# Kernel tuning notes

Hardware: AMD Instinct MI355X
Metric: run time of the kernel (lower is better)

## Reference

```python
import jax, jax.numpy as jnp
import numpy as np
from jax import lax

INF = 1e6  # stand-in for infinity; INF**2 = 1e12 fits comfortably in fp32


def _boundary_3x3(targets):
    """morphological_gradient(size=(3,3)) > 0 on int label maps [B,H,W].
    scipy default mode='reflect' with pad width 1 == edge padding."""
    B, H, W = targets.shape
    p = jnp.pad(targets, ((0, 0), (1, 1), (1, 1)), mode='edge')
    patches = jnp.stack([p[:, i:i + H, j:j + W]
                         for i in range(3) for j in range(3)], axis=0)
    return (patches.max(0) - patches.min(0)) > 0  # [B,H,W] bool


def _row_dist(boundary):
    """Per-row 1D distance (in column index) to nearest boundary pixel. [B,H,W] float."""
    B, H, W = boundary.shape
    bT = jnp.moveaxis(boundary, 2, 0)  # [W,B,H]

    def step(c, b):
        c = jnp.where(b, 0.0, jnp.minimum(c + 1.0, INF))
        return c, c

    init = jnp.full((B, H), INF, dtype=jnp.float32)
    _, fwd = lax.scan(step, init, bT)
    _, bwd = lax.scan(step, init, bT[::-1])
    g = jnp.minimum(fwd, bwd[::-1])  # [W,B,H]
    return jnp.moveaxis(g, 0, 2)  # [B,H,W]


def _edt(boundary):
    """Exact 2D Euclidean distance transform to the boundary set (separable form):
    d(i,j)^2 = min_k ( (i-k)^2 + g(k,j)^2 )."""
    B, H, W = boundary.shape
    g2 = _row_dist(boundary) ** 2  # [B,H,W]
    ii = jnp.arange(H, dtype=jnp.float32)
    dk2 = (ii[:, None] - ii[None, :]) ** 2  # [H_i, H_k]
    # [B, H_i, H_k, W] -> min over k
    d2 = jnp.min(dk2[None, :, :, None] + g2[:, None, :, :], axis=2)
    return jnp.sqrt(d2)


def boundary_weight(targets, sigma):
    boundary = _boundary_3x3(targets)
    dist = _edt(boundary)
    w = jnp.exp(-dist / sigma)
    has_b = boundary.any(axis=(1, 2))[:, None, None]
    return jnp.where(has_b, w, 1.0)  # all-ones map if no boundary


def setup_inputs() -> dict:
    key = jax.random.key(0)
    k1, k2 = jax.random.split(key)
    B, C, H, W = 8, 19, 256, 256
    inputs = jax.random.normal(k1, (B, C, H, W), dtype=jnp.float32)
    targets = jax.random.randint(k2, (B, H, W), 0, C, dtype=jnp.int32)
    return {"inputs": inputs, "targets": targets}


def reference(inputs, targets):
    sigma = 5.0
    logp = jax.nn.log_softmax(inputs, axis=1)  # [B,C,H,W]
    ce = -jnp.take_along_axis(logp, targets[:, None, :, :], axis=1)[:, 0]  # [B,H,W]
    w = boundary_weight(targets, sigma)
    return (ce * w).mean()
```

## Files before the change

### kernel.cpp

```cpp
#include <hip/hip_runtime.h>

#define BB 8
#define CC 19
#define HH 256
#define WW 256
#define HWW 65536
#define IT 8
#define BIGF 3.0e12f


__global__ __launch_bounds__(256) void k_bnd_ce(
    const float* __restrict__ x, const int* __restrict__ tgt,
    float* __restrict__ g2, float* __restrict__ ce,
    int* __restrict__ rowany, float* __restrict__ out)
{
    const int blk = blockIdx.x;
    const int b   = blk >> 6;
    const int i0  = (blk & 63) << 2;
    const int j   = threadIdx.x;

    __shared__ int trow[6][WW];
    __shared__ int bflag[4][WW];
    __shared__ int s_any;

    if (blk == 0 && j == 0) out[0] = 0.0f;
    if (j == 0) s_any = 0;

    const int* tbase = tgt + b * HWW;
#pragma unroll
    for (int rr = 0; rr < 6; ++rr) {
        int hh = min(max(i0 - 1 + rr, 0), HH - 1);
        trow[rr][j] = tbase[hh * WW + j];
    }
    __syncthreads();

    const int r  = j >> 6;
    const int c0 = (j & 63) << 2;
    const int h  = i0 + r;

    int anyb = 0;
#pragma unroll
    for (int t = 0; t < 4; ++t) {
        int c = c0 + t;
        int cm = max(c - 1, 0), cp = min(c + 1, WW - 1);
        int mx = trow[r][cm], mn = mx;
#pragma unroll
        for (int rr = 0; rr < 3; ++rr) {
            int a0 = trow[r + rr][cm], a1 = trow[r + rr][c], a2 = trow[r + rr][cp];
            mx = max(mx, max(a0, max(a1, a2)));
            mn = min(mn, min(a0, min(a1, a2)));
        }
        int bnd = (mx != mn) ? 1 : 0;
        bflag[r][c] = bnd;
        anyb |= bnd;
    }
    unsigned long long msk = __ballot(anyb);
    if ((j & 63) == 0 && msk) s_any = 1;
    __syncthreads();
    if (j == 0) rowany[blk] = s_any;

    float4 g4;
    float* gp = (float*)&g4;
#pragma unroll
    for (int t = 0; t < 4; ++t) {
        int c = c0 + t;
        float mind = 1e6f;
        for (int d = 0; d < WW; ++d) {
            int lo = c - d, hi = c + d;
            if ((lo >= 0 && bflag[r][lo]) || (hi < WW && bflag[r][hi])) {
                mind = (float)d; break;
            }
        }
        gp[t] = mind * mind;
    }
    *(float4*)(g2 + (size_t)(b * HH + h) * WW + c0) = g4;

    const float* px = x + ((size_t)(b * CC) * HH + h) * WW + c0;
    float4 s4 = make_float4(0.f, 0.f, 0.f, 0.f);
#pragma unroll
    for (int c = 0; c < CC; ++c) {
        float4 v = *(const float4*)(px + (size_t)c * HWW);
        s4.x += expf(v.x); s4.y += expf(v.y);
        s4.z += expf(v.z); s4.w += expf(v.w);
    }
    const int t0 = trow[r + 1][c0],     t1 = trow[r + 1][c0 + 1],
              t2 = trow[r + 1][c0 + 2], t3 = trow[r + 1][c0 + 3];
    float4 c4;
    c4.x = logf(s4.x) - px[(size_t)t0 * HWW + 0];
    c4.y = logf(s4.y) - px[(size_t)t1 * HWW + 1];
    c4.z = logf(s4.z) - px[(size_t)t2 * HWW + 2];
    c4.w = logf(s4.w) - px[(size_t)t3 * HWW + 3];
    *(float4*)(ce + (size_t)(b * HH + h) * WW + c0) = c4;
}

__global__ __launch_bounds__(256) void k_edt_red(
    const float* __restrict__ g2, const float* __restrict__ ce,
    const int* __restrict__ rowany, float* __restrict__ out)
{
    const int b  = blockIdx.x >> 5;
    const int i0 = (blockIdx.x & 31) * IT;
    const int j  = threadIdx.x;

    __shared__ int s_has;
    __shared__ float wsum[4];
    if (j == 0) s_has = 0;
    int ra = (j < 64) ? rowany[b * 64 + j] : 0;
    unsigned long long mk = __ballot(ra != 0);
    __syncthreads();
    if ((j & 63) == 0 && mk) s_has = 1;
    __syncthreads();
    const int has = s_has;

    float md[IT];
#pragma unroll
    for (int r = 0; r < IT; ++r) md[r] = BIGF;
    const float* gcol = g2 + (size_t)b * HWW + j;
    const int c0 = i0 + 4;
    for (int d0 = 0; d0 < HH; d0 += 4) {
        float gl[4], gr[4];
        int   kl[4], kr[4];
#pragma unroll
        for (int t = 0; t < 4; ++t) {
            int d = d0 + t;
            kl[t] = c0 - d; kr[t] = c0 + d;
            gl[t] = (kl[t] >= 0 && kl[t] < HH) ? gcol[(size_t)kl[t] * WW] : BIGF;
            gr[t] = (kr[t] >= 0 && kr[t] < HH) ? gcol[(size_t)kr[t] * WW] : BIGF;
        }
#pragma unroll
        for (int t = 0; t < 4; ++t) {
#pragma unroll
            for (int r = 0; r < IT; ++r) {
                float dl = (float)(i0 + r - kl[t]);
                float dr = (float)(i0 + r - kr[t]);
                md[r] = fminf(md[r], fmaf(dl, dl, gl[t]));
                md[r] = fminf(md[r], fmaf(dr, dr, gr[t]));
            }
        }
        float bm = md[0];
#pragma unroll
        for (int r = 1; r < IT; ++r) bm = fmaxf(bm, md[r]);
        float fut = (float)(d0 * d0);
        if (fut > bm) break;
    }

    float acc = 0.0f;
#pragma unroll
    for (int r = 0; r < IT; ++r) {
        float dist = sqrtf(md[r]);
        float w = has ? expf(-dist / 5.0f) : 1.0f;
        acc += ce[((size_t)b * HH + i0 + r) * WW + j] * w;
    }

    for (int off = 32; off > 0; off >>= 1)
        acc += __shfl_down(acc, off, 64);
    const int lane = j & 63, wid = j >> 6;
    if (lane == 0) wsum[wid] = acc;
    __syncthreads();
    if (j == 0) {
        float tot = wsum[0] + wsum[1] + wsum[2] + wsum[3];
        atomicAdd(out, tot * (1.0f / (float)(BB * HWW)));
    }
}

extern "C" void kernel_launch(void* const* d_in, const int* in_sizes, int n_in,
                              void* d_out, int out_size, void* d_ws, size_t ws_size,
                              hipStream_t stream) {
    const float* x   = (const float*)d_in[0];
    const int*   tgt = (const int*)d_in[1];
    float*       out = (float*)d_out;

    char* ws = (char*)d_ws;
    float* g2     = (float*)ws;
    float* ce     = (float*)(ws + (size_t)BB * HWW * sizeof(float));
    int*   rowany = (int*)  (ws + (size_t)2 * BB * HWW * sizeof(float));

    k_bnd_ce <<<BB * (HH / 4), 256, 0, stream>>>(x, tgt, g2, ce, rowany, out);
    k_edt_red<<<BB * (HH / IT), 256, 0, stream>>>(g2, ce, rowany, out);
}
```

Baseline: 86.99 us.

## Double threads in boundary/CE kernel and prefetch logits before boundary work

```diff
diff --git a/kernel.cpp b/kernel.cpp
--- a/kernel.cpp
+++ b/kernel.cpp
@@ -9,7 +9,7 @@
 #define BIGF 3.0e12f
 
 
-__global__ __launch_bounds__(256) void k_bnd_ce(
+__global__ __launch_bounds__(512, 4) void k_bnd_ce(
     const float* __restrict__ x, const int* __restrict__ tgt,
     float* __restrict__ g2, float* __restrict__ ce,
     int* __restrict__ rowany, float* __restrict__ out)
@@ -26,21 +26,36 @@
     if (blk == 0 && j == 0) out[0] = 0.0f;
     if (j == 0) s_any = 0;
 
+    const int r  = j >> 7;
+    const int c0 = (j & 127) << 1;
+    const int h  = i0 + r;
+
     const int* tbase = tgt + b * HWW;
+    int tv[3];
 #pragma unroll
-    for (int rr = 0; rr < 6; ++rr) {
+    for (int k = 0; k < 3; ++k) {
+        int idx = j + (k << 9);
+        int rr = idx >> 8, cc = idx & 255;
         int hh = min(max(i0 - 1 + rr, 0), HH - 1);
-        trow[rr][j] = tbase[hh * WW + j];
+        tv[k] = tbase[hh * WW + cc];
+    }
+
+    const float* px = x + ((size_t)(b * CC) * HH + h) * WW + c0;
+    float2 v[CC];
+#pragma unroll
+    for (int c = 0; c < CC; ++c)
+        v[c] = *(const float2*)(px + (size_t)c * HWW);
+
+#pragma unroll
+    for (int k = 0; k < 3; ++k) {
+        int idx = j + (k << 9);
+        trow[idx >> 8][idx & 255] = tv[k];
     }
     __syncthreads();
 
-    const int r  = j >> 6;
-    const int c0 = (j & 63) << 2;
-    const int h  = i0 + r;
-
     int anyb = 0;
 #pragma unroll
-    for (int t = 0; t < 4; ++t) {
+    for (int t = 0; t < 2; ++t) {
         int c = c0 + t;
         int cm = max(c - 1, 0), cp = min(c + 1, WW - 1);
         int mx = trow[r][cm], mn = mx;
@@ -59,10 +74,9 @@
     __syncthreads();
     if (j == 0) rowany[blk] = s_any;
 
-    float4 g4;
-    float* gp = (float*)&g4;
+    float gv[2];
 #pragma unroll
-    for (int t = 0; t < 4; ++t) {
+    for (int t = 0; t < 2; ++t) {
         int c = c0 + t;
         float mind = 1e6f;
         for (int d = 0; d < WW; ++d) {
@@ -71,26 +85,20 @@
                 mind = (float)d; break;
             }
         }
-        gp[t] = mind * mind;
+        gv[t] = mind * mind;
     }
-    *(float4*)(g2 + (size_t)(b * HH + h) * WW + c0) = g4;
+    *(float2*)(g2 + (size_t)(b * HH + h) * WW + c0) = make_float2(gv[0], gv[1]);
 
-    const float* px = x + ((size_t)(b * CC) * HH + h) * WW + c0;
-    float4 s4 = make_float4(0.f, 0.f, 0.f, 0.f);
+    const int t0 = trow[r + 1][c0], t1 = trow[r + 1][c0 + 1];
+    float sx = 0.0f, sy = 0.0f, xv0 = 0.0f, xv1 = 0.0f;
 #pragma unroll
     for (int c = 0; c < CC; ++c) {
-        float4 v = *(const float4*)(px + (size_t)c * HWW);
-        s4.x += expf(v.x); s4.y += expf(v.y);
-        s4.z += expf(v.z); s4.w += expf(v.w);
+        sx += expf(v[c].x); sy += expf(v[c].y);
+        xv0 = (c == t0) ? v[c].x : xv0;
+        xv1 = (c == t1) ? v[c].y : xv1;
     }
-    const int t0 = trow[r + 1][c0],     t1 = trow[r + 1][c0 + 1],
-              t2 = trow[r + 1][c0 + 2], t3 = trow[r + 1][c0 + 3];
-    float4 c4;
-    c4.x = logf(s4.x) - px[(size_t)t0 * HWW + 0];
-    c4.y = logf(s4.y) - px[(size_t)t1 * HWW + 1];
-    c4.z = logf(s4.z) - px[(size_t)t2 * HWW + 2];
-    c4.w = logf(s4.w) - px[(size_t)t3 * HWW + 3];
-    *(float4*)(ce + (size_t)(b * HH + h) * WW + c0) = c4;
+    *(float2*)(ce + (size_t)(b * HH + h) * WW + c0) =
+        make_float2(logf(sx) - xv0, logf(sy) - xv1);
 }
 
 __global__ __launch_bounds__(256) void k_edt_red(
@@ -174,6 +182,6 @@
     float* ce     = (float*)(ws + (size_t)BB * HWW * sizeof(float));
     int*   rowany = (int*)  (ws + (size_t)2 * BB * HWW * sizeof(float));
 
-    k_bnd_ce <<<BB * (HH / 4), 256, 0, stream>>>(x, tgt, g2, ce, rowany, out);
+    k_bnd_ce <<<BB * (HH / 4), 512, 0, stream>>>(x, tgt, g2, ce, rowany, out);
     k_edt_red<<<BB * (HH / IT), 256, 0, stream>>>(g2, ce, rowany, out);
 }
```

Result: no change. 87.30 us (+0.4%).

## Prefetch logits before boundary work and shrink blocks in both kernels

Applied to the files above, without the earlier changes.

```diff
diff --git a/kernel.cpp b/kernel.cpp
--- a/kernel.cpp
+++ b/kernel.cpp
@@ -5,38 +5,53 @@
 #define HH 256
 #define WW 256
 #define HWW 65536
-#define IT 8
+#define IT 4
 #define BIGF 3.0e12f
 
 
-__global__ __launch_bounds__(256) void k_bnd_ce(
+__global__ __launch_bounds__(128, 4) void k_bnd_ce(
     const float* __restrict__ x, const int* __restrict__ tgt,
     float* __restrict__ g2, float* __restrict__ ce,
     int* __restrict__ rowany, float* __restrict__ out)
 {
     const int blk = blockIdx.x;
-    const int b   = blk >> 6;
-    const int i0  = (blk & 63) << 2;
+    const int b   = blk >> 7;
+    const int i0  = (blk & 127) << 1;
     const int j   = threadIdx.x;
 
-    __shared__ int trow[6][WW];
-    __shared__ int bflag[4][WW];
+    __shared__ int trow[4][WW];
+    __shared__ int bflag[2][WW];
     __shared__ int s_any;
 
     if (blk == 0 && j == 0) out[0] = 0.0f;
     if (j == 0) s_any = 0;
 
-    const int* tbase = tgt + b * HWW;
-#pragma unroll
-    for (int rr = 0; rr < 6; ++rr) {
-        int hh = min(max(i0 - 1 + rr, 0), HH - 1);
-        trow[rr][j] = tbase[hh * WW + j];
-    }
-    __syncthreads();
-
     const int r  = j >> 6;
     const int c0 = (j & 63) << 2;
     const int h  = i0 + r;
+
+    const int* tbase = tgt + b * HWW;
+    int tv[8];
+#pragma unroll
+    for (int k = 0; k < 8; ++k) {
+        int idx = j + (k << 7);
+        int rr = idx >> 8, cc = idx & 255;
+        int hh = min(max(i0 - 1 + rr, 0), HH - 1);
+        tv[k] = tbase[hh * WW + cc];
+    }
+
+    const float* px = x + ((size_t)(b * CC) * HH + h) * WW + c0;
+    float4 v[CC];
+#pragma unroll
+    for (int c = 0; c < CC; ++c)
+        v[c] = *(const float4*)(px + (size_t)c * HWW);
+
+#pragma unroll
+    for (int k = 0; k < 8; ++k) {
+        int idx = j + (k << 7);
+        trow[idx >> 8][idx & 255] = tv[k];
+    }
+    __syncthreads();
 
     int anyb = 0;
 #pragma unroll
@@ -75,21 +90,24 @@
     }
     *(float4*)(g2 + (size_t)(b * HH + h) * WW + c0) = g4;
 
-    const float* px = x + ((size_t)(b * CC) * HH + h) * WW + c0;
+    const int t0 = trow[r + 1][c0],     t1 = trow[r + 1][c0 + 1],
+              t2 = trow[r + 1][c0 + 2], t3 = trow[r + 1][c0 + 3];
     float4 s4 = make_float4(0.f, 0.f, 0.f, 0.f);
+    float xv0 = 0.f, xv1 = 0.f, xv2 = 0.f, xv3 = 0.f;
 #pragma unroll
     for (int c = 0; c < CC; ++c) {
-        float4 v = *(const float4*)(px + (size_t)c * HWW);
-        s4.x += expf(v.x); s4.y += expf(v.y);
-        s4.z += expf(v.z); s4.w += expf(v.w);
+        s4.x += expf(v[c].x); s4.y += expf(v[c].y);
+        s4.z += expf(v[c].z); s4.w += expf(v[c].w);
+        xv0 = (c == t0) ? v[c].x : xv0;
+        xv1 = (c == t1) ? v[c].y : xv1;
+        xv2 = (c == t2) ? v[c].z : xv2;
+        xv3 = (c == t3) ? v[c].w : xv3;
     }
-    const int t0 = trow[r + 1][c0],     t1 = trow[r + 1][c0 + 1],
-              t2 = trow[r + 1][c0 + 2], t3 = trow[r + 1][c0 + 3];
     float4 c4;
-    c4.x = logf(s4.x) - px[(size_t)t0 * HWW + 0];
-    c4.y = logf(s4.y) - px[(size_t)t1 * HWW + 1];
-    c4.z = logf(s4.z) - px[(size_t)t2 * HWW + 2];
-    c4.w = logf(s4.w) - px[(size_t)t3 * HWW + 3];
+    c4.x = logf(s4.x) - xv0;
+    c4.y = logf(s4.y) - xv1;
+    c4.z = logf(s4.z) - xv2;
+    c4.w = logf(s4.w) - xv3;
     *(float4*)(ce + (size_t)(b * HH + h) * WW + c0) = c4;
 }
 
@@ -97,14 +115,14 @@
     const float* __restrict__ g2, const float* __restrict__ ce,
     const int* __restrict__ rowany, float* __restrict__ out)
 {
-    const int b  = blockIdx.x >> 5;
-    const int i0 = (blockIdx.x & 31) * IT;
+    const int b  = blockIdx.x >> 6;
+    const int i0 = (blockIdx.x & 63) * IT;
     const int j  = threadIdx.x;
 
     __shared__ int s_has;
     __shared__ float wsum[4];
     if (j == 0) s_has = 0;
-    int ra = (j < 64) ? rowany[b * 64 + j] : 0;
+    int ra = (j < 128) ? rowany[b * 128 + j] : 0;
     unsigned long long mk = __ballot(ra != 0);
     __syncthreads();
     if ((j & 63) == 0 && mk) s_has = 1;
@@ -115,7 +133,7 @@
 #pragma unroll
     for (int r = 0; r < IT; ++r) md[r] = BIGF;
     const float* gcol = g2 + (size_t)b * HWW + j;
-    const int c0 = i0 + 4;
+    const int c0 = i0 + 2;
     for (int d0 = 0; d0 < HH; d0 += 4) {
         float gl[4], gr[4];
         int   kl[4], kr[4];
@@ -174,6 +192,6 @@
     float* ce     = (float*)(ws + (size_t)BB * HWW * sizeof(float));
     int*   rowany = (int*)  (ws + (size_t)2 * BB * HWW * sizeof(float));
 
-    k_bnd_ce <<<BB * (HH / 4), 256, 0, stream>>>(x, tgt, g2, ce, rowany, out);
+    k_bnd_ce <<<BB * (HH / 2), 128, 0, stream>>>(x, tgt, g2, ce, rowany, out);
     k_edt_red<<<BB * (HH / IT), 256, 0, stream>>>(g2, ce, rowany, out);
 }
```

Measured after the change: 93.42 us. +7.4%, slower.

## Fuse boundary/CE and EDT reduction into one cooperative grid-synced kernel

Applied to the files above, without the earlier changes.

```diff
diff --git a/kernel.cpp b/kernel.cpp
--- a/kernel.cpp
+++ b/kernel.cpp
@@ -1,13 +1,164 @@
 #include <hip/hip_runtime.h>
+#include <hip/hip_cooperative_groups.h>
+
+namespace cg = cooperative_groups;
 
 #define BB 8
 #define CC 19
 #define HH 256
 #define WW 256
 #define HWW 65536
-#define IT 8
 #define BIGF 3.0e12f
-
+#define SENT 1.0e11f
+
+
+__global__ __launch_bounds__(256) void k_fused(
+    const float* __restrict__ x, const int* __restrict__ tgt,
+    float* __restrict__ g2, float* __restrict__ out)
+{
+    const int blk = blockIdx.x;
+    const int b   = blk >> 6;
+    const int i0  = (blk & 63) << 2;
+    const int j   = threadIdx.x;
+
+    __shared__ int   trow[6][WW];
+    __shared__ int   bflag[4][WW];
+    __shared__ float gsh[4][WW];
+    __shared__ float wsum[4];
+
+    if (blk == 0 && j == 0) out[0] = 0.0f;
+
+    const int* tbase = tgt + b * HWW;
+#pragma unroll
+    for (int rr = 0; rr < 6; ++rr) {
+        int hh = min(max(i0 - 1 + rr, 0), HH - 1);
+        trow[rr][j] = tbase[hh * WW + j];
+    }
+
+    const int r  = j >> 6;
+    const int c0 = (j & 63) << 2;
+    const int h  = i0 + r;
+
+    const float* px = x + ((size_t)(b * CC) * HH + h) * WW + c0;
+    float4 v[CC];
+#pragma unroll
+    for (int c = 0; c < CC; ++c)
+        v[c] = *(const float4*)(px + (size_t)c * HWW);
+
+    __syncthreads();
+
+#pragma unroll
+    for (int t = 0; t < 4; ++t) {
+        int c = c0 + t;
+        int cm = max(c - 1, 0), cp = min(c + 1, WW - 1);
+        int mx = trow[r][cm], mn = mx;
+#pragma unroll
+        for (int rr = 0; rr < 3; ++rr) {
+            int a0 = trow[r + rr][cm], a1 = trow[r + rr][c], a2 = trow[r + rr][cp];
+            mx = max(mx, max(a0, max(a1, a2)));
+            mn = min(mn, min(a0, min(a1, a2)));
+        }
+        bflag[r][c] = (mx != mn) ? 1 : 0;
+    }
+    __syncthreads();
+
+    float4 g4;
+    float* gp = (float*)&g4;
+#pragma unroll
+    for (int t = 0; t < 4; ++t) {
+        int c = c0 + t;
+        float mind = 1e6f;
+        for (int d = 0; d < WW; ++d) {
+            int lo = c - d, hi = c + d;
+            if ((lo >= 0 && bflag[r][lo]) || (hi < WW && bflag[r][hi])) {
+                mind = (float)d; break;
+            }
+        }
+        gp[t] = mind * mind;
+    }
+    *(float4*)&gsh[r][c0] = g4;
+    *(float4*)(g2 + (size_t)(b * HH + h) * WW + c0) = g4;
+
+    const int t0 = trow[r + 1][c0],     t1 = trow[r + 1][c0 + 1],
+              t2 = trow[r + 1][c0 + 2], t3 = trow[r + 1][c0 + 3];
+    float4 s4 = make_float4(0.f, 0.f, 0.f, 0.f);
+    float xv0 = 0.f, xv1 = 0.f, xv2 = 0.f, xv3 = 0.f;
+#pragma unroll
+    for (int c = 0; c < CC; ++c) {
+        s4.x += expf(v[c].x); s4.y += expf(v[c].y);
+        s4.z += expf(v[c].z); s4.w += expf(v[c].w);
+        xv0 = (c == t0) ? v[c].x : xv0;
+        xv1 = (c == t1) ? v[c].y : xv1;
+        xv2 = (c == t2) ? v[c].z : xv2;
+        xv3 = (c == t3) ? v[c].w : xv3;
+    }
+    const float ce0 = logf(s4.x) - xv0, ce1 = logf(s4.y) - xv1,
+                ce2 = logf(s4.z) - xv2, ce3 = logf(s4.w) - xv3;
+
+    __threadfence();
+    cg::this_grid().sync();
+
+    float md0 = gp[0], md1 = gp[1], md2 = gp[2], md3 = gp[3];
+    const float* gimg = g2 + (size_t)b * HWW;
+#pragma unroll
+    for (int t = 1; t <= 3; ++t) {
+        const float ft2 = (float)(t * t);
+        float4 gu, gd;
+        int ru = r - t, ku = h - t;
+        if (ru >= 0)        gu = *(const float4*)&gsh[ru][c0];
+        else if (ku >= 0)   gu = *(const float4*)(gimg + (size_t)ku * WW + c0);
+        else                gu = make_float4(BIGF, BIGF, BIGF, BIGF);
+        int rd = r + t, kd = h + t;
+        if (rd <= 3)        gd = *(const float4*)&gsh[rd][c0];
+        else if (kd < HH)   gd = *(const float4*)(gimg + (size_t)kd * WW + c0);
+        else                gd = make_float4(BIGF, BIGF, BIGF, BIGF);
+        md0 = fminf(md0, fminf(gu.x, gd.x) + ft2);
+        md1 = fminf(md1, fminf(gu.y, gd.y) + ft2);
+        md2 = fminf(md2, fminf(gu.z, gd.z) + ft2);
+        md3 = fminf(md3, fminf(gu.w, gd.w) + ft2);
+    }
+    float bm = fmaxf(fmaxf(md0, md1), fmaxf(md2, md3));
+    if (!(16.0f > bm)) {
+        for (int d0 = 4; d0 < HH; d0 += 4) {
+#pragma unroll
+            for (int t = 0; t < 4; ++t) {
+                int d = d0 + t;
+                float fd2 = (float)(d * d);
+                int ku = h - d, kd = h + d;
+                float4 gu = (ku >= 0) ? *(const float4*)(gimg + (size_t)ku * WW + c0)
+                                      : make_float4(BIGF, BIGF, BIGF, BIGF);
+                float4 gd = (kd < HH) ? *(const float4*)(gimg + (size_t)kd * WW + c0)
+                                      : make_float4(BIGF, BIGF, BIGF, BIGF);
+                md0 = fminf(md0, fminf(gu.x, gd.x) + fd2);
+                md1 = fminf(md1, fminf(gu.y, gd.y) + fd2);
+                md2 = fminf(md2, fminf(gu.z, gd.z) + fd2);
+                md3 = fminf(md3, fminf(gu.w, gd.w) + fd2);
+            }
+            bm = fmaxf(fmaxf(md0, md1), fmaxf(md2, md3));
+            float nxt = (float)((d0 + 4) * (d0 + 4));
+            if (nxt > bm) break;
+        }
+    }
+
+    float acc;
+    {
+        float w0 = (md0 < SENT) ? expf(-sqrtf(md0) / 5.0f) : 1.0f;
+        float w1 = (md1 < SENT) ? expf(-sqrtf(md1) / 5.0f) : 1.0f;
+        float w2 = (md2 < SENT) ? expf(-sqrtf(md2) / 5.0f) : 1.0f;
+        float w3 = (md3 < SENT) ? expf(-sqrtf(md3) / 5.0f) : 1.0f;
+        acc = ce0 * w0; acc += ce1 * w1; acc += ce2 * w2; acc += ce3 * w3;
+    }
+
+    for (int off = 32; off > 0; off >>= 1)
+        acc += __shfl_down(acc, off, 64);
+    const int lane = j & 63, wid = j >> 6;
+    if (lane == 0) wsum[wid] = acc;
+    __syncthreads();
+    if (j == 0) {
+        float tot = wsum[0] + wsum[1] + wsum[2] + wsum[3];
+        atomicAdd(out, tot * (1.0f / (float)(BB * HWW)));
+    }
+}
 
 __global__ __launch_bounds__(256) void k_bnd_ce(
     const float* __restrict__ x, const int* __restrict__ tgt,
@@ -79,9 +230,9 @@
     float4 s4 = make_float4(0.f, 0.f, 0.f, 0.f);
 #pragma unroll
     for (int c = 0; c < CC; ++c) {
-        float4 v = *(const float4*)(px + (size_t)c * HWW);
-        s4.x += expf(v.x); s4.y += expf(v.y);
-        s4.z += expf(v.z); s4.w += expf(v.w);
+        float4 vv = *(const float4*)(px + (size_t)c * HWW);
+        s4.x += expf(vv.x); s4.y += expf(vv.y);
+        s4.z += expf(vv.z); s4.w += expf(vv.w);
     }
     const int t0 = trow[r + 1][c0],     t1 = trow[r + 1][c0 + 1],
               t2 = trow[r + 1][c0 + 2], t3 = trow[r + 1][c0 + 3];
@@ -93,6 +244,7 @@
     *(float4*)(ce + (size_t)(b * HH + h) * WW + c0) = c4;
 }
 
+#define IT 8
 __global__ __launch_bounds__(256) void k_edt_red(
     const float* __restrict__ g2, const float* __restrict__ ce,
     const int* __restrict__ rowany, float* __restrict__ out)
@@ -174,6 +326,12 @@
     float* ce     = (float*)(ws + (size_t)BB * HWW * sizeof(float));
     int*   rowany = (int*)  (ws + (size_t)2 * BB * HWW * sizeof(float));
 
-    k_bnd_ce <<<BB * (HH / 4), 256, 0, stream>>>(x, tgt, g2, ce, rowany, out);
-    k_edt_red<<<BB * (HH / IT), 256, 0, stream>>>(g2, ce, rowany, out);
+    void* args[] = { (void*)&x, (void*)&tgt, (void*)&g2, (void*)&out };
+    hipError_t e = hipLaunchCooperativeKernel((const void*)k_fused,
+                                              dim3(BB * (HH / 4)), dim3(256),
+                                              args, 0, stream);
+    if (e != hipSuccess) {
+        k_bnd_ce <<<BB * (HH / 4), 256, 0, stream>>>(x, tgt, g2, ce, rowany, out);
+        k_edt_red<<<BB * (HH / IT), 256, 0, stream>>>(g2, ce, rowany, out);
+    }
 }
```

Result: slower. 186.6 us (+114.5%).
